# Kernel tuning notes

Measured on AMD Instinct MI355X. Metric: run time of the kernel, lower is better.

## Reference

```python
import jax, jax.numpy as jnp
import numpy as np

IN_F = 512
OUT_F = 512
NOISE_DIM = 128
BATCH = 512
OUT_DIM = IN_F * OUT_F + OUT_F  # 262656
PRIOR_STD = 1.0
PRIOR_SCALE = 1.0
POSTERIOR_SCALE = 1.0


def setup_inputs() -> dict:
    key = jax.random.key(0)
    k1, k2, k3, k4, k5, k6 = jax.random.split(key, 6)
    x = jax.random.normal(k1, (BATCH, IN_F), dtype=jnp.float32)
    prior_x = jax.random.normal(k2, (BATCH, IN_F), dtype=jnp.float32)
    hyper_noise = jax.random.normal(k3, (BATCH, NOISE_DIM), dtype=jnp.float32)
    # hypermodel = nn.Linear(noise_dim, out_dim): kaiming-uniform-ish init approximated by uniform
    bound = 1.0 / np.sqrt(NOISE_DIM)
    hW = jax.random.uniform(k4, (OUT_DIM, NOISE_DIM), jnp.float32, -bound, bound)
    hb = jax.random.uniform(k5, (OUT_DIM,), jnp.float32, -bound, bound)
    # PriorHyperLinear: row-normalized gaussian weight scaled by prior_std (eye), zero bias (prior_mean=0)
    pW = jax.random.normal(k6, (OUT_DIM, NOISE_DIM), dtype=jnp.float32)
    pW = PRIOR_STD * pW / jnp.linalg.norm(pW, axis=1, keepdims=True)
    pb = jnp.zeros((OUT_DIM,), dtype=jnp.float32)
    return {"x": x, "prior_x": prior_x, "hyper_noise": hyper_noise,
            "hW": hW, "hb": hb, "pW": pW, "pb": pb}


def _base_forward(x, params):
    # params: [B, in*out + out] -> per-sample weight [B, in, out], bias [B, out]
    weight = params[:, : IN_F * OUT_F].reshape(-1, IN_F, OUT_F)
    bias = params[:, IN_F * OUT_F:]  # [B, out]
    # bmm(x[:,None,:], weight) + bias -> [B, out]
    return jnp.einsum("bi,bio->bo", x, weight) + bias


def reference(x, prior_x, hyper_noise, hW, hb, pW, pb):
    params = hyper_noise @ hW.T + hb  # [B, out_dim]
    out = _base_forward(x, params)
    prior_params = hyper_noise @ pW.T + pb
    prior_out = _base_forward(prior_x, prior_params)
    return out * POSTERIOR_SCALE + prior_out * PRIOR_SCALE
```

## Files before the change

### kernel.cpp

```cpp
#include <hip/hip_runtime.h>
#include <hip/hip_fp16.h>

#define BATCH 512
#define INF   512
#define OUTF  512
#define ND    128
#define WPART 262144

typedef __attribute__((ext_vector_type(8))) _Float16 half8;
typedef __attribute__((ext_vector_type(2))) _Float16 half2v;
typedef __attribute__((ext_vector_type(4))) float    f32x4;

__device__ inline half8 cvt8(float4 a, float4 b) {
  half2v h0 = __builtin_bit_cast(half2v, __builtin_amdgcn_cvt_pkrtz(a.x, a.y));
  half2v h1 = __builtin_bit_cast(half2v, __builtin_amdgcn_cvt_pkrtz(a.z, a.w));
  half2v h2 = __builtin_bit_cast(half2v, __builtin_amdgcn_cvt_pkrtz(b.x, b.y));
  half2v h3 = __builtin_bit_cast(half2v, __builtin_amdgcn_cvt_pkrtz(b.z, b.w));
  half8 r = { h0[0], h0[1], h1[0], h1[1], h2[0], h2[1], h3[0], h3[1] };
  return r;
}

__global__ void __launch_bounds__(256) transpose_kernel(
    const float* __restrict__ x, const float* __restrict__ px,
    float* __restrict__ xt) {
  __shared__ float t[32][33];
  const float* src = blockIdx.z ? px : x;
  float* dst = xt + ((size_t)blockIdx.z << 18);
  const int bi = blockIdx.x * 32, bb = blockIdx.y * 32;
  const int tx = threadIdx.x & 31, ty = threadIdx.x >> 5;
  #pragma unroll
  for (int r = 0; r < 32; r += 8)
    t[ty + r][tx] = src[(size_t)(bb + ty + r) * 512 + bi + tx];
  __syncthreads();
  #pragma unroll
  for (int r = 0; r < 32; r += 8)
    dst[(size_t)(bi + ty + r) * 512 + bb + tx] = t[tx][ty + r];
}

__global__ void __launch_bounds__(256) tail_kernel(
    const float* __restrict__ hn, const float* __restrict__ hW,
    const float* __restrict__ pW, float* __restrict__ TT) {
  const int bt = blockIdx.x & 7;
  const int bg = blockIdx.x >> 3;
  __shared__ float wsum[64][132];
  __shared__ float hs[32][132];
  {
    int r = threadIdx.x >> 2, seg = threadIdx.x & 3;
    const float4* h4 = (const float4*)(hW + (((size_t)(WPART + bt*64 + r)) << 7) + seg*32);
    const float4* p4 = (const float4*)(pW + (((size_t)(WPART + bt*64 + r)) << 7) + seg*32);
    #pragma unroll
    for (int qq = 0; qq < 8; ++qq) {
      float4 a = h4[qq], b = p4[qq];
      float* d = &wsum[r][seg*32 + qq*4];
      d[0]=a.x+b.x; d[1]=a.y+b.y; d[2]=a.z+b.z; d[3]=a.w+b.w;
    }
    int bb = threadIdx.x >> 3, ch = threadIdx.x & 7;
    const float4* hh = (const float4*)(hn + (((size_t)(bg*32 + bb)) << 7) + ch*16);
    #pragma unroll
    for (int qq = 0; qq < 4; ++qq) {
      float4 a = hh[qq];
      float* d = &hs[bb][ch*16 + qq*4];
      d[0]=a.x; d[1]=a.y; d[2]=a.z; d[3]=a.w;
    }
  }
  __syncthreads();
  const int ol = threadIdx.x & 63, b0 = (threadIdx.x >> 6) * 8;
  float a[8] = {};
  for (int n = 0; n < 128; n += 4) {
    float4 wv = *(const float4*)&wsum[ol][n];
    #pragma unroll
    for (int r = 0; r < 8; ++r) {
      float4 hv = *(const float4*)&hs[b0 + r][n];
      a[r] += hv.x*wv.x + hv.y*wv.y + hv.z*wv.z + hv.w*wv.w;
    }
  }
  #pragma unroll
  for (int r = 0; r < 8; ++r)
    TT[(((size_t)(bg*32 + b0 + r)) << 9) + bt*64 + ol] = a[r];
}

__global__ void __launch_bounds__(1024, 4) gemm_kernel(
    const float* __restrict__ xt, const float* __restrict__ hn,
    const float* __restrict__ hW, const float* __restrict__ pW,
    float* __restrict__ P, int S) {
  const int tid = threadIdx.x;
  const int lane = tid & 63, w = tid >> 6;
  const int l15 = lane & 15, j = lane >> 4;
  const int wrow0 = w << 5;

  const int n0 = blockIdx.x << 6;
  const int q  = blockIdx.y;
  const int spb  = S >> 3;
  const int half = S >> 1;
  const int part = q / half;
  const int rem  = q % half;
  const int nh   = rem / spb;
  const int irange = 512 / spb;
  const int i0   = (rem % spb) * irange;
  const int nst  = irange >> 1;
  const float* srcW = part ? pW : hW;
  const float* xtp  = xt + ((size_t)part << 18);
  const int woff = nh << 5;

  __shared__ half8 ldsW[2][512];

  f32x4 acc[2][4] = {};

  const int o_s = tid >> 4;
  const int g_s = tid & 15;
  const int isub_s = g_s >> 3;
  const size_t colbase = (((size_t)(n0 + o_s)) << 7) + woff + ((g_s & 7) << 2);
  const int wdst = (o_s << 7) + (((((g_s >> 1)) ^ (o_s & 7)) << 4) | ((g_s & 1) << 3));

  half8 hnf[2];
  #pragma unroll
  for (int m = 0; m < 2; ++m) {
    int row = wrow0 + m * 16 + l15;
    const float4* hp = (const float4*)(hn + ((size_t)row << 7) + woff + (j << 3));
    hnf[m] = cvt8(hp[0], hp[1]);
  }

  auto loadW = [&](int ph, float4& rw) {
    int i = i0 + 2 * ph + isub_s;
    rw = *(const float4*)(srcW + ((size_t)i << 16) + colbase);
  };
  auto writeW = [&](int buf, float4 rw) {
    unsigned u0 = __builtin_bit_cast(unsigned, __builtin_amdgcn_cvt_pkrtz(rw.x, rw.y));
    unsigned u1 = __builtin_bit_cast(unsigned, __builtin_amdgcn_cvt_pkrtz(rw.z, rw.w));
    uint2 u; u.x = u0; u.y = u1;
    *(uint2*)((char*)&ldsW[buf][0] + wdst) = u;
  };
  auto loadX = [&](int ph, float4& xq) {
    const float* g = xtp + (((size_t)(i0 + 2 * ph)) << 9) + wrow0 + l15;
    xq.x = g[0];
    xq.y = g[16];
    xq.z = g[512];
    xq.w = g[528];
  };
  auto compute = [&](int buf, float4 xq) {
    const char* bW = (const char*)&ldsW[buf][0];
    #pragma unroll
    for (int kk = 0; kk < 2; ++kk) {
      half8 af[2], bf[4];
      _Float16 t0 = (_Float16)(kk ? xq.z : xq.x);
      _Float16 t1 = (_Float16)(kk ? xq.w : xq.y);
      half8 xb0 = { t0, t0, t0, t0, t0, t0, t0, t0 };
      half8 xb1 = { t1, t1, t1, t1, t1, t1, t1, t1 };
      af[0] = hnf[0] * xb0;
      af[1] = hnf[1] * xb1;
      #pragma unroll
      for (int nn = 0; nn < 4; ++nn) {
        int byte = (((nn << 4) + l15) << 7) + (((((kk << 2) + j)) ^ (l15 & 7)) << 4);
        bf[nn] = *(const half8*)(bW + byte);
      }
      __builtin_amdgcn_s_setprio(1);
      #pragma unroll
      for (int m = 0; m < 2; ++m)
        #pragma unroll
        for (int nn = 0; nn < 4; ++nn)
          acc[m][nn] = __builtin_amdgcn_mfma_f32_16x16x32_f16(
              af[m], bf[nn], acc[m][nn], 0, 0, 0);
      __builtin_amdgcn_s_setprio(0);
    }
  };

  float4 rw0, rw1, rw2, rw3, xq0, xq1, xq2, xq3;
  loadW(0, rw0); loadX(0, xq0);
  loadW(1, rw1); loadX(1, xq1);
  loadW(2, rw2); loadX(2, xq2);
  loadW(3, rw3); loadX(3, xq3);
  writeW(0, rw0);

#define PHASE(p, RWCUR, XQCUR, RWNEXT, BUF)                                \
  {                                                                        \
    asm volatile("s_waitcnt lgkmcnt(0)" ::: "memory");                     \
    __builtin_amdgcn_s_barrier();                                          \
    if ((p) + 4 < nst) loadW((p) + 4, RWCUR);                              \
    compute(BUF, XQCUR);                                                   \
    if ((p) + 4 < nst) loadX((p) + 4, XQCUR);                              \
    if ((p) + 1 < nst) writeW(BUF ^ 1, RWNEXT);                            \
  }

  for (int p = 0; p < nst; p += 4) {
    PHASE(p + 0, rw0, xq0, rw1, 0)
    PHASE(p + 1, rw1, xq1, rw2, 1)
    PHASE(p + 2, rw2, xq2, rw3, 0)
    PHASE(p + 3, rw3, xq3, rw0, 1)
  }
#undef PHASE

  float* outp = P + ((size_t)q << 18);
  #pragma unroll
  for (int m = 0; m < 2; ++m) {
    int row = wrow0 + m * 16 + (j << 2);
    #pragma unroll
    for (int nn = 0; nn < 4; ++nn) {
      int col = n0 + (nn << 4) + l15;
      float* op = outp + (size_t)row * OUTF + col;
      op[0]    = acc[m][nn][0];
      op[512]  = acc[m][nn][1];
      op[1024] = acc[m][nn][2];
      op[1536] = acc[m][nn][3];
    }
  }
}

__global__ void __launch_bounds__(256) finish_kernel(
    const float* __restrict__ P, const float* __restrict__ x,
    const float* __restrict__ hb, const float* __restrict__ TT,
    float* __restrict__ out, int S) {
  const int o  = blockIdx.x * 256 + threadIdx.x;
  const int b0 = blockIdx.y * 2;
  __shared__ float xs[2][512];
  #pragma unroll
  for (int t = 0; t < 4; ++t) {
    int idx = threadIdx.x + t * 256;
    xs[idx >> 9][idx & 511] = x[((size_t)(b0 + (idx >> 9)) << 9) + (idx & 511)];
  }
  __syncthreads();

  const float bias = hb[WPART + o];
  float a0 = bias, a1 = bias;
  #pragma unroll 16
  for (int i = 0; i < 512; ++i) {
    float hv = hb[(i << 9) + o];
    a0 += xs[0][i] * hv;
    a1 += xs[1][i] * hv;
  }
  a0 += TT[((size_t)b0 << 9) + o];
  a1 += TT[((size_t)(b0 + 1) << 9) + o];

  const float* P0 = P + ((size_t)b0 << 9) + o;
  const float* P1 = P0 + 512;
  float t00 = 0, t01 = 0, t10 = 0, t11 = 0;
  #pragma unroll 4
  for (int k = 0; k < S; k += 2) {
    t00 += P0[(size_t)(k)     << 18];
    t01 += P0[(size_t)(k + 1) << 18];
    t10 += P1[(size_t)(k)     << 18];
    t11 += P1[(size_t)(k + 1) << 18];
  }
  out[((size_t)b0 << 9) + o]       = a0 + t00 + t01;
  out[((size_t)(b0 + 1) << 9) + o] = a1 + t10 + t11;
}

extern "C" void kernel_launch(void* const* d_in, const int* in_sizes, int n_in,
                              void* d_out, int out_size, void* d_ws, size_t ws_size,
                              hipStream_t stream) {
  const float* x  = (const float*)d_in[0];
  const float* px = (const float*)d_in[1];
  const float* hn = (const float*)d_in[2];
  const float* hW = (const float*)d_in[3];
  const float* hb = (const float*)d_in[4];
  const float* pW = (const float*)d_in[5];
  float* out = (float*)d_out;
  float* xt  = (float*)d_ws;
  float* TT  = xt + (1 << 19);
  float* P   = TT + (1 << 18);

  int S = 32;
  while (S > 8 && (((size_t)(3 + S)) << 20) > ws_size) S >>= 1;

  transpose_kernel<<<dim3(16, 16, 2), 256, 0, stream>>>(x, px, xt);
  tail_kernel<<<dim3(128), 256, 0, stream>>>(hn, hW, pW, TT);
  gemm_kernel<<<dim3(8, S), dim3(1024), 0, stream>>>(xt, hn, hW, pW, P, S);
  finish_kernel<<<dim3(2, 256), dim3(256), 0, stream>>>(P, x, hb, TT, out, S);
}
```

Measured before the change: 116.3 us.

## Retile MFMA GEMM to 4x2 warp fragments with four i-steps per stage

Each warp now covers a 64-row by 32-column tile (4x2 MFMA fragments) instead of 32x64, and every pipeline stage consumes four input rows i instead of two, which halves the number of barrier-separated stages. The W staging buffer doubles to 1024 half8 per buffer with a new swizzle, and each thread loads 8 contiguous floats per stage. The prefetch depth drops from four to two register stages. The intent is to cut barrier and LDS-read overhead per MFMA, at the cost of more registers and less latency hiding for global loads.

```diff
diff --git a/kernel.cpp b/kernel.cpp
--- a/kernel.cpp
+++ b/kernel.cpp
@@ -19,6 +19,8 @@
   half8 r = { h0[0], h0[1], h1[0], h1[1], h2[0], h2[1], h3[0], h3[1] };
   return r;
 }
+
+struct XQ { float4 k0, k1, k2, k3; };
 
 __global__ void __launch_bounds__(256) transpose_kernel(
     const float* __restrict__ x, const float* __restrict__ px,
@@ -86,7 +88,8 @@
   const int tid = threadIdx.x;
   const int lane = tid & 63, w = tid >> 6;
   const int l15 = lane & 15, j = lane >> 4;
-  const int wrow0 = w << 5;
+  const int wm = w >> 1, wn = w & 1;
+  const int wrow0 = wm << 6;
 
   const int n0 = blockIdx.x << 6;
   const int q  = blockIdx.y;
@@ -97,105 +100,111 @@
   const int nh   = rem / spb;
   const int irange = 512 / spb;
   const int i0   = (rem % spb) * irange;
-  const int nst  = irange >> 1;
+  const int nst  = irange >> 2;
   const float* srcW = part ? pW : hW;
   const float* xtp  = xt + ((size_t)part << 18);
   const int woff = nh << 5;
 
-  __shared__ half8 ldsW[2][512];
-
-  f32x4 acc[2][4] = {};
-
-  const int o_s = tid >> 4;
-  const int g_s = tid & 15;
-  const int isub_s = g_s >> 3;
-  const size_t colbase = (((size_t)(n0 + o_s)) << 7) + woff + ((g_s & 7) << 2);
-  const int wdst = (o_s << 7) + (((((g_s >> 1)) ^ (o_s & 7)) << 4) | ((g_s & 1) << 3));
-
-  half8 hnf[2];
-  #pragma unroll
-  for (int m = 0; m < 2; ++m) {
+  __shared__ half8 ldsW[2][1024];
+
+  f32x4 acc[4][2] = {};
+
+  const int col_s = tid >> 4;
+  const int c_s   = tid & 15;
+  const int isub_s = c_s >> 2;
+  const int nloc_s = (c_s & 3) << 3;
+  const int swz_s  = (c_s & 8) | ((c_s & 7) ^ (col_s & 7));
+  const int wbyte  = (col_s << 8) + (swz_s << 4);
+
+  half8 hnf[4];
+  #pragma unroll
+  for (int m = 0; m < 4; ++m) {
     int row = wrow0 + m * 16 + l15;
     const float4* hp = (const float4*)(hn + ((size_t)row << 7) + woff + (j << 3));
     hnf[m] = cvt8(hp[0], hp[1]);
   }
 
-  auto loadW = [&](int ph, float4& rw) {
-    int i = i0 + 2 * ph + isub_s;
-    rw = *(const float4*)(srcW + ((size_t)i << 16) + colbase);
-  };
-  auto writeW = [&](int buf, float4 rw) {
-    unsigned u0 = __builtin_bit_cast(unsigned, __builtin_amdgcn_cvt_pkrtz(rw.x, rw.y));
-    unsigned u1 = __builtin_bit_cast(unsigned, __builtin_amdgcn_cvt_pkrtz(rw.z, rw.w));
-    uint2 u; u.x = u0; u.y = u1;
-    *(uint2*)((char*)&ldsW[buf][0] + wdst) = u;
-  };
-  auto loadX = [&](int ph, float4& xq) {
-    const float* g = xtp + (((size_t)(i0 + 2 * ph)) << 9) + wrow0 + l15;
-    xq.x = g[0];
-    xq.y = g[16];
-    xq.z = g[512];
-    xq.w = g[528];
-  };
-  auto compute = [&](int buf, float4 xq) {
+  auto loadW = [&](int ph, float4& ra, float4& rb) {
+    int i = i0 + 4 * ph + isub_s;
+    const float* g = srcW + (((size_t)((i << 9) + n0 + col_s)) << 7) + woff + nloc_s;
+    ra = *(const float4*)g;
+    rb = *(const float4*)(g + 4);
+  };
+  auto writeW = [&](int buf, float4 ra, float4 rb) {
+    *(half8*)((char*)&ldsW[buf][0] + wbyte) = cvt8(ra, rb);
+  };
+  auto loadX = [&](int ph, XQ& xq) {
+    const float* g = xtp + (((size_t)(i0 + 4 * ph)) << 9) + wrow0 + l15;
+    xq.k0 = make_float4(g[0],        g[16],        g[32],        g[48]);
+    xq.k1 = make_float4(g[512],      g[528],       g[544],       g[560]);
+    xq.k2 = make_float4(g[1024],     g[1040],      g[1056],      g[1072]);
+    xq.k3 = make_float4(g[1536],     g[1552],      g[1568],      g[1584]);
+  };
+  auto compute = [&](int buf, const XQ& xq) {
     const char* bW = (const char*)&ldsW[buf][0];
     #pragma unroll
-    for (int kk = 0; kk < 2; ++kk) {
-      half8 af[2], bf[4];
-      _Float16 t0 = (_Float16)(kk ? xq.z : xq.x);
-      _Float16 t1 = (_Float16)(kk ? xq.w : xq.y);
-      half8 xb0 = { t0, t0, t0, t0, t0, t0, t0, t0 };
-      half8 xb1 = { t1, t1, t1, t1, t1, t1, t1, t1 };
-      af[0] = hnf[0] * xb0;
-      af[1] = hnf[1] * xb1;
+    for (int kk = 0; kk < 4; ++kk) {
+      float4 xk = kk == 0 ? xq.k0 : kk == 1 ? xq.k1 : kk == 2 ? xq.k2 : xq.k3;
+      half8 bf[2];
       #pragma unroll
-      for (int nn = 0; nn < 4; ++nn) {
-        int byte = (((nn << 4) + l15) << 7) + (((((kk << 2) + j)) ^ (l15 & 7)) << 4);
-        bf[nn] = *(const half8*)(bW + byte);
+      for (int nn = 0; nn < 2; ++nn) {
+        int col = (wn << 5) + (nn << 4) + l15;
+        int ch  = (kk << 2) + j;
+        int swz = (ch & 8) | ((ch & 7) ^ (col & 7));
+        bf[nn] = *(const half8*)(bW + (col << 8) + (swz << 4));
       }
+      _Float16 t0 = (_Float16)xk.x, t1 = (_Float16)xk.y;
+      _Float16 t2 = (_Float16)xk.z, t3 = (_Float16)xk.w;
+      half8 xb0 = { t0,t0,t0,t0,t0,t0,t0,t0 };
+      half8 xb1 = { t1,t1,t1,t1,t1,t1,t1,t1 };
+      half8 xb2 = { t2,t2,t2,t2,t2,t2,t2,t2 };
+      half8 xb3 = { t3,t3,t3,t3,t3,t3,t3,t3 };
+      half8 af0 = hnf[0] * xb0;
+      half8 af1 = hnf[1] * xb1;
+      half8 af2 = hnf[2] * xb2;
+      half8 af3 = hnf[3] * xb3;
       __builtin_amdgcn_s_setprio(1);
       #pragma unroll
-      for (int m = 0; m < 2; ++m)
-        #pragma unroll
-        for (int nn = 0; nn < 4; ++nn)
-          acc[m][nn] = __builtin_amdgcn_mfma_f32_16x16x32_f16(
-              af[m], bf[nn], acc[m][nn], 0, 0, 0);
+      for (int nn = 0; nn < 2; ++nn) {
+        acc[0][nn] = __builtin_amdgcn_mfma_f32_16x16x32_f16(af0, bf[nn], acc[0][nn], 0, 0, 0);
+        acc[1][nn] = __builtin_amdgcn_mfma_f32_16x16x32_f16(af1, bf[nn], acc[1][nn], 0, 0, 0);
+        acc[2][nn] = __builtin_amdgcn_mfma_f32_16x16x32_f16(af2, bf[nn], acc[2][nn], 0, 0, 0);
+        acc[3][nn] = __builtin_amdgcn_mfma_f32_16x16x32_f16(af3, bf[nn], acc[3][nn], 0, 0, 0);
+      }
       __builtin_amdgcn_s_setprio(0);
     }
   };
 
-  float4 rw0, rw1, rw2, rw3, xq0, xq1, xq2, xq3;
-  loadW(0, rw0); loadX(0, xq0);
-  loadW(1, rw1); loadX(1, xq1);
-  loadW(2, rw2); loadX(2, xq2);
-  loadW(3, rw3); loadX(3, xq3);
-  writeW(0, rw0);
-
-#define PHASE(p, RWCUR, XQCUR, RWNEXT, BUF)                                \
-  {                                                                        \
-    asm volatile("s_waitcnt lgkmcnt(0)" ::: "memory");                     \
-    __builtin_amdgcn_s_barrier();                                          \
-    if ((p) + 4 < nst) loadW((p) + 4, RWCUR);                              \
-    compute(BUF, XQCUR);                                                   \
-    if ((p) + 4 < nst) loadX((p) + 4, XQCUR);                              \
-    if ((p) + 1 < nst) writeW(BUF ^ 1, RWNEXT);                            \
-  }
-
-  for (int p = 0; p < nst; p += 4) {
-    PHASE(p + 0, rw0, xq0, rw1, 0)
-    PHASE(p + 1, rw1, xq1, rw2, 1)
-    PHASE(p + 2, rw2, xq2, rw3, 0)
-    PHASE(p + 3, rw3, xq3, rw0, 1)
-  }
-#undef PHASE
+  float4 rwA0, rwA1, rwB0, rwB1;
+  XQ xA, xB;
+  loadW(0, rwA0, rwA1);
+  loadX(0, xA);
+  loadW(1, rwB0, rwB1);
+  writeW(0, rwA0, rwA1);
+
+  for (int p = 0; p < nst; p += 2) {
+    asm volatile("s_waitcnt lgkmcnt(0)" ::: "memory");
+    __builtin_amdgcn_s_barrier();
+    if (p + 2 < nst) loadW(p + 2, rwA0, rwA1);
+    if (p + 1 < nst) loadX(p + 1, xB);
+    compute(0, xA);
+    if (p + 1 < nst) writeW(1, rwB0, rwB1);
+
+    asm volatile("s_waitcnt lgkmcnt(0)" ::: "memory");
+    __builtin_amdgcn_s_barrier();
+    if (p + 3 < nst) loadW(p + 3, rwB0, rwB1);
+    if (p + 2 < nst) loadX(p + 2, xA);
+    if (p + 1 < nst) compute(1, xB);
+    if (p + 2 < nst) writeW(0, rwA0, rwA1);
+  }
 
   float* outp = P + ((size_t)q << 18);
   #pragma unroll
-  for (int m = 0; m < 2; ++m) {
+  for (int m = 0; m < 4; ++m) {
     int row = wrow0 + m * 16 + (j << 2);
     #pragma unroll
-    for (int nn = 0; nn < 4; ++nn) {
-      int col = n0 + (nn << 4) + l15;
+    for (int nn = 0; nn < 2; ++nn) {
+      int col = n0 + (wn << 5) + (nn << 4) + l15;
       float* op = outp + (size_t)row * OUTF + col;
       op[0]    = acc[m][nn][0];
       op[512]  = acc[m][nn][1];
```

Result: slower. 133.3 us (+14.6%).

## Retile gemm to 512-thread blocks with 64-row warps and interleaved x layout

Applied to the files above, without the earlier changes.

The GEMM block shrinks from 1024 to 512 threads. Each warp now covers 64 batch rows by 32 output columns, using 4x2 MFMA tiles instead of 2x4, and twice as many blocks are launched along the column dimension. The transpose kernel now writes x in pairs of consecutive i as float2, so each x load fetches both k-steps with one 8-byte access, and the x prefetch depth drops from 4 to 2 stages. This cuts the number of scalar x loads and registers held, at the cost of loading the W tile from HBM twice as often relative to rows, since each block covers fewer columns.

```diff
diff --git a/kernel.cpp b/kernel.cpp
--- a/kernel.cpp
+++ b/kernel.cpp
@@ -20,12 +20,14 @@
   return r;
 }
 
+struct XR { float2 m0, m1, m2, m3; };
+
 __global__ void __launch_bounds__(256) transpose_kernel(
     const float* __restrict__ x, const float* __restrict__ px,
     float* __restrict__ xt) {
   __shared__ float t[32][33];
   const float* src = blockIdx.z ? px : x;
-  float* dst = xt + ((size_t)blockIdx.z << 18);
+  float2* dst = (float2*)(xt + ((size_t)blockIdx.z << 18));
   const int bi = blockIdx.x * 32, bb = blockIdx.y * 32;
   const int tx = threadIdx.x & 31, ty = threadIdx.x >> 5;
   #pragma unroll
@@ -33,8 +35,11 @@
     t[ty + r][tx] = src[(size_t)(bb + ty + r) * 512 + bi + tx];
   __syncthreads();
   #pragma unroll
-  for (int r = 0; r < 32; r += 8)
-    dst[(size_t)(bi + ty + r) * 512 + bb + tx] = t[tx][ty + r];
+  for (int r = 0; r < 16; r += 8) {
+    int ipl = ty + r;
+    float2 v; v.x = t[tx][2 * ipl]; v.y = t[tx][2 * ipl + 1];
+    dst[(size_t)((bi >> 1) + ipl) * 512 + bb + tx] = v;
+  }
 }
 
 __global__ void __launch_bounds__(256) tail_kernel(
@@ -79,16 +84,16 @@
     TT[(((size_t)(bg*32 + b0 + r)) << 9) + bt*64 + ol] = a[r];
 }
 
-__global__ void __launch_bounds__(1024, 4) gemm_kernel(
+__global__ void __launch_bounds__(512, 4) gemm_kernel(
     const float* __restrict__ xt, const float* __restrict__ hn,
     const float* __restrict__ hW, const float* __restrict__ pW,
     float* __restrict__ P, int S) {
   const int tid = threadIdx.x;
   const int lane = tid & 63, w = tid >> 6;
   const int l15 = lane & 15, j = lane >> 4;
-  const int wrow0 = w << 5;
-
-  const int n0 = blockIdx.x << 6;
+  const int wrow0 = w << 6;
+
+  const int n0 = blockIdx.x << 5;
   const int q  = blockIdx.y;
   const int spb  = S >> 3;
   const int half = S >> 1;
@@ -99,12 +104,13 @@
   const int i0   = (rem % spb) * irange;
   const int nst  = irange >> 1;
   const float* srcW = part ? pW : hW;
-  const float* xtp  = xt + ((size_t)part << 18);
+  const float2* xt2p = (const float2*)(xt + ((size_t)part << 18));
+  const int ip0 = i0 >> 1;
   const int woff = nh << 5;
 
-  __shared__ half8 ldsW[2][512];
-
-  f32x4 acc[2][4] = {};
+  __shared__ half8 ldsW[2][256];
+
+  f32x4 acc[4][2] = {};
 
   const int o_s = tid >> 4;
   const int g_s = tid & 15;
@@ -112,9 +118,9 @@
   const size_t colbase = (((size_t)(n0 + o_s)) << 7) + woff + ((g_s & 7) << 2);
   const int wdst = (o_s << 7) + (((((g_s >> 1)) ^ (o_s & 7)) << 4) | ((g_s & 1) << 3));
 
-  half8 hnf[2];
-  #pragma unroll
-  for (int m = 0; m < 2; ++m) {
+  half8 hnf[4];
+  #pragma unroll
+  for (int m = 0; m < 4; ++m) {
     int row = wrow0 + m * 16 + l15;
     const float4* hp = (const float4*)(hn + ((size_t)row << 7) + woff + (j << 3));
     hnf[m] = cvt8(hp[0], hp[1]);
@@ -130,71 +136,75 @@
     uint2 u; u.x = u0; u.y = u1;
     *(uint2*)((char*)&ldsW[buf][0] + wdst) = u;
   };
-  auto loadX = [&](int ph, float4& xq) {
-    const float* g = xtp + (((size_t)(i0 + 2 * ph)) << 9) + wrow0 + l15;
-    xq.x = g[0];
-    xq.y = g[16];
-    xq.z = g[512];
-    xq.w = g[528];
-  };
-  auto compute = [&](int buf, float4 xq) {
+  auto loadX = [&](int ph, XR& xq) {
+    const float2* g = xt2p + (((size_t)(ip0 + ph)) << 9) + wrow0 + l15;
+    xq.m0 = g[0]; xq.m1 = g[16]; xq.m2 = g[32]; xq.m3 = g[48];
+  };
+  auto compute = [&](int buf, const XR& xq) {
     const char* bW = (const char*)&ldsW[buf][0];
     #pragma unroll
     for (int kk = 0; kk < 2; ++kk) {
-      half8 af[2], bf[4];
-      _Float16 t0 = (_Float16)(kk ? xq.z : xq.x);
-      _Float16 t1 = (_Float16)(kk ? xq.w : xq.y);
-      half8 xb0 = { t0, t0, t0, t0, t0, t0, t0, t0 };
-      half8 xb1 = { t1, t1, t1, t1, t1, t1, t1, t1 };
-      af[0] = hnf[0] * xb0;
-      af[1] = hnf[1] * xb1;
+      half8 bf[2];
       #pragma unroll
-      for (int nn = 0; nn < 4; ++nn) {
-        int byte = (((nn << 4) + l15) << 7) + (((((kk << 2) + j)) ^ (l15 & 7)) << 4);
+      for (int nn = 0; nn < 2; ++nn) {
+        int col = (nn << 4) + l15;
+        int byte = (col << 7) + (((((kk << 2) + j)) ^ (l15 & 7)) << 4);
         bf[nn] = *(const half8*)(bW + byte);
       }
+      _Float16 t0 = (_Float16)(kk ? xq.m0.y : xq.m0.x);
+      _Float16 t1 = (_Float16)(kk ? xq.m1.y : xq.m1.x);
+      _Float16 t2 = (_Float16)(kk ? xq.m2.y : xq.m2.x);
+      _Float16 t3 = (_Float16)(kk ? xq.m3.y : xq.m3.x);
+      half8 xb0 = { t0,t0,t0,t0,t0,t0,t0,t0 };
+      half8 xb1 = { t1,t1,t1,t1,t1,t1,t1,t1 };
+      half8 xb2 = { t2,t2,t2,t2,t2,t2,t2,t2 };
+      half8 xb3 = { t3,t3,t3,t3,t3,t3,t3,t3 };
+      half8 af0 = hnf[0] * xb0;
+      half8 af1 = hnf[1] * xb1;
+      half8 af2 = hnf[2] * xb2;
+      half8 af3 = hnf[3] * xb3;
       __builtin_amdgcn_s_setprio(1);
       #pragma unroll
-      for (int m = 0; m < 2; ++m)
-        #pragma unroll
-        for (int nn = 0; nn < 4; ++nn)
-          acc[m][nn] = __builtin_amdgcn_mfma_f32_16x16x32_f16(
-              af[m], bf[nn], acc[m][nn], 0, 0, 0);
+      for (int nn = 0; nn < 2; ++nn) {
+        acc[0][nn] = __builtin_amdgcn_mfma_f32_16x16x32_f16(af0, bf[nn], acc[0][nn], 0, 0, 0);
+        acc[1][nn] = __builtin_amdgcn_mfma_f32_16x16x32_f16(af1, bf[nn], acc[1][nn], 0, 0, 0);
+        acc[2][nn] = __builtin_amdgcn_mfma_f32_16x16x32_f16(af2, bf[nn], acc[2][nn], 0, 0, 0);
+        acc[3][nn] = __builtin_amdgcn_mfma_f32_16x16x32_f16(af3, bf[nn], acc[3][nn], 0, 0, 0);
+      }
       __builtin_amdgcn_s_setprio(0);
     }
   };
 
-  float4 rw0, rw1, rw2, rw3, xq0, xq1, xq2, xq3;
-  loadW(0, rw0); loadX(0, xq0);
-  loadW(1, rw1); loadX(1, xq1);
-  loadW(2, rw2); loadX(2, xq2);
-  loadW(3, rw3); loadX(3, xq3);
+  float4 rw0, rw1, rw2, rw3;
+  XR xqA, xqB;
+  loadW(0, rw0); loadW(1, rw1); loadW(2, rw2); loadW(3, rw3);
+  loadX(0, xqA); loadX(1, xqB);
   writeW(0, rw0);
 
-#define PHASE(p, RWCUR, XQCUR, RWNEXT, BUF)                                \
+#define PH(p, RWCUR, RWNEXT, BUF, XQ)                                      \
   {                                                                        \
     asm volatile("s_waitcnt lgkmcnt(0)" ::: "memory");                     \
     __builtin_amdgcn_s_barrier();                                          \
     if ((p) + 4 < nst) loadW((p) + 4, RWCUR);                              \
-    compute(BUF, XQCUR);                                                   \
-    if ((p) + 4 < nst) loadX((p) + 4, XQCUR);                              \
+    compute(BUF, XQ);                                                      \
+    if ((p) + 2 < nst) loadX((p) + 2, XQ);                                 \
     if ((p) + 1 < nst) writeW(BUF ^ 1, RWNEXT);                            \
   }
 
   for (int p = 0; p < nst; p += 4) {
-    PHASE(p + 0, rw0, xq0, rw1, 0)
-    PHASE(p + 1, rw1, xq1, rw2, 1)
-    PHASE(p + 2, rw2, xq2, rw3, 0)
-    PHASE(p + 3, rw3, xq3, rw0, 1)
-  }
-#undef PHASE
+    PH(p + 0, rw0, rw1, 0, xqA)
+    PH(p + 1, rw1, rw2, 1, xqB)
+    PH(p + 2, rw2, rw3, 0, xqA)
+    PH(p + 3, rw3, rw0, 1, xqB)
+  }
+#undef PH
 
   float* outp = P + ((size_t)q << 18);
   #pragma unroll
-  for (int m = 0; m < 2; ++m) {
+  for (int m = 0; m < 4; ++m) {
     int row = wrow0 + m * 16 + (j << 2);
     #pragma unroll
-    for (int nn = 0; nn < 4; ++nn) {
+    for (int nn = 0; nn < 2; ++nn) {
       int col = n0 + (nn << 4) + l15;
       float* op = outp + (size_t)row * OUTF + col;
       op[0]    = acc[m][nn][0];
@@ -263,6 +273,6 @@
 
   transpose_kernel<<<dim3(16, 16, 2), 256, 0, stream>>>(x, px, xt);
   tail_kernel<<<dim3(128), 256, 0, stream>>>(hn, hW, pW, TT);
-  gemm_kernel<<<dim3(8, S), dim3(1024), 0, stream>>>(xt, hn, hW, pW, P, S);
+  gemm_kernel<<<dim3(16, S), dim3(512), 0, stream>>>(xt, hn, hW, pW, P, S);
   finish_kernel<<<dim3(2, 256), dim3(256), 0, stream>>>(P, x, hb, TT, out, S);
 }
```

After: 145.8 us. 25.3% more time.

## Double per-stage K depth in gemm pipeline and pair x columns in transpose

Applied to the files above, without the earlier changes.

Each pipeline stage in the GEMM now processes four input rows instead of two. This halves the number of barrier-synchronized stages and doubles the LDS buffer. The transposed x layout is changed to store pairs of i values as float2, so each thread loads x with fewer, wider reads. The cost is more registers held per stage (two float4 W loads per prefetch slot) and more LDS, which may reduce occupancy under the 1024-thread launch bound.

```diff
diff --git a/kernel.cpp b/kernel.cpp
--- a/kernel.cpp
+++ b/kernel.cpp
@@ -20,12 +20,15 @@
   return r;
 }
 
+struct WR  { float4 a, b; };
+struct XR2 { float2 a0, a1, b0, b1; };
+
 __global__ void __launch_bounds__(256) transpose_kernel(
     const float* __restrict__ x, const float* __restrict__ px,
     float* __restrict__ xt) {
   __shared__ float t[32][33];
   const float* src = blockIdx.z ? px : x;
-  float* dst = xt + ((size_t)blockIdx.z << 18);
+  float2* dst = (float2*)(xt + ((size_t)blockIdx.z << 18));
   const int bi = blockIdx.x * 32, bb = blockIdx.y * 32;
   const int tx = threadIdx.x & 31, ty = threadIdx.x >> 5;
   #pragma unroll
@@ -33,8 +36,11 @@
     t[ty + r][tx] = src[(size_t)(bb + ty + r) * 512 + bi + tx];
   __syncthreads();
   #pragma unroll
-  for (int r = 0; r < 32; r += 8)
-    dst[(size_t)(bi + ty + r) * 512 + bb + tx] = t[tx][ty + r];
+  for (int r = 0; r < 16; r += 8) {
+    int ipl = ty + r;
+    float2 v; v.x = t[tx][2 * ipl]; v.y = t[tx][2 * ipl + 1];
+    dst[(size_t)((bi >> 1) + ipl) * 512 + bb + tx] = v;
+  }
 }
 
 __global__ void __launch_bounds__(256) tail_kernel(
@@ -97,12 +103,13 @@
   const int nh   = rem / spb;
   const int irange = 512 / spb;
   const int i0   = (rem % spb) * irange;
-  const int nst  = irange >> 1;
+  const int nst  = irange >> 2;
   const float* srcW = part ? pW : hW;
-  const float* xtp  = xt + ((size_t)part << 18);
+  const float2* xt2p = (const float2*)(xt + ((size_t)part << 18));
+  const int ip0 = i0 >> 1;
   const int woff = nh << 5;
 
-  __shared__ half8 ldsW[2][512];
+  __shared__ half8 ldsW[2][1024];
 
   f32x4 acc[2][4] = {};
 
@@ -110,7 +117,7 @@
   const int g_s = tid & 15;
   const int isub_s = g_s >> 3;
   const size_t colbase = (((size_t)(n0 + o_s)) << 7) + woff + ((g_s & 7) << 2);
-  const int wdst = (o_s << 7) + (((((g_s >> 1)) ^ (o_s & 7)) << 4) | ((g_s & 1) << 3));
+  const int wdstI = (((((g_s >> 1)) ^ (o_s & 7)) << 4) | ((g_s & 1) << 3));
 
   half8 hnf[2];
   #pragma unroll
@@ -120,37 +127,45 @@
     hnf[m] = cvt8(hp[0], hp[1]);
   }
 
-  auto loadW = [&](int ph, float4& rw) {
-    int i = i0 + 2 * ph + isub_s;
-    rw = *(const float4*)(srcW + ((size_t)i << 16) + colbase);
-  };
-  auto writeW = [&](int buf, float4 rw) {
-    unsigned u0 = __builtin_bit_cast(unsigned, __builtin_amdgcn_cvt_pkrtz(rw.x, rw.y));
-    unsigned u1 = __builtin_bit_cast(unsigned, __builtin_amdgcn_cvt_pkrtz(rw.z, rw.w));
-    uint2 u; u.x = u0; u.y = u1;
-    *(uint2*)((char*)&ldsW[buf][0] + wdst) = u;
-  };
-  auto loadX = [&](int ph, float4& xq) {
-    const float* g = xtp + (((size_t)(i0 + 2 * ph)) << 9) + wrow0 + l15;
-    xq.x = g[0];
-    xq.y = g[16];
-    xq.z = g[512];
-    xq.w = g[528];
-  };
-  auto compute = [&](int buf, float4 xq) {
+  auto loadW = [&](int ph, WR& r) {
+    int iA = i0 + 4 * ph + isub_s;
+    r.a = *(const float4*)(srcW + ((size_t)iA << 16) + colbase);
+    r.b = *(const float4*)(srcW + ((size_t)(iA + 2) << 16) + colbase);
+  };
+  auto writeW = [&](int buf, const WR& r) {
+    unsigned ua0 = __builtin_bit_cast(unsigned, __builtin_amdgcn_cvt_pkrtz(r.a.x, r.a.y));
+    unsigned ua1 = __builtin_bit_cast(unsigned, __builtin_amdgcn_cvt_pkrtz(r.a.z, r.a.w));
+    unsigned ub0 = __builtin_bit_cast(unsigned, __builtin_amdgcn_cvt_pkrtz(r.b.x, r.b.y));
+    unsigned ub1 = __builtin_bit_cast(unsigned, __builtin_amdgcn_cvt_pkrtz(r.b.z, r.b.w));
+    char* base = (char*)&ldsW[buf][0] + (o_s << 8) + wdstI;
+    uint2 u0; u0.x = ua0; u0.y = ua1;
+    uint2 u1; u1.x = ub0; u1.y = ub1;
+    *(uint2*)base         = u0;
+    *(uint2*)(base + 128) = u1;
+  };
+  auto loadX = [&](int ph, XR2& xq) {
+    const float2* g = xt2p + (((size_t)(ip0 + 2 * ph)) << 9) + wrow0 + l15;
+    xq.a0 = g[0]; xq.a1 = g[16];
+    xq.b0 = g[512]; xq.b1 = g[528];
+  };
+  auto compute = [&](int buf, const XR2& xq) {
     const char* bW = (const char*)&ldsW[buf][0];
     #pragma unroll
-    for (int kk = 0; kk < 2; ++kk) {
+    for (int kk = 0; kk < 4; ++kk) {
       half8 af[2], bf[4];
-      _Float16 t0 = (_Float16)(kk ? xq.z : xq.x);
-      _Float16 t1 = (_Float16)(kk ? xq.w : xq.y);
-      half8 xb0 = { t0, t0, t0, t0, t0, t0, t0, t0 };
-      half8 xb1 = { t1, t1, t1, t1, t1, t1, t1, t1 };
+      float2 xm0 = (kk & 2) ? xq.b0 : xq.a0;
+      float2 xm1 = (kk & 2) ? xq.b1 : xq.a1;
+      _Float16 t0 = (_Float16)((kk & 1) ? xm0.y : xm0.x);
+      _Float16 t1 = (_Float16)((kk & 1) ? xm1.y : xm1.x);
+      half8 xb0 = { t0,t0,t0,t0,t0,t0,t0,t0 };
+      half8 xb1 = { t1,t1,t1,t1,t1,t1,t1,t1 };
       af[0] = hnf[0] * xb0;
       af[1] = hnf[1] * xb1;
       #pragma unroll
       for (int nn = 0; nn < 4; ++nn) {
-        int byte = (((nn << 4) + l15) << 7) + (((((kk << 2) + j)) ^ (l15 & 7)) << 4);
+        int col  = (nn << 4) + l15;
+        int byte = (col << 8) + ((kk >> 1) << 7)
+                 + (((((kk & 1) << 2) + j) ^ (l15 & 7)) << 4);
         bf[nn] = *(const half8*)(bW + byte);
       }
       __builtin_amdgcn_s_setprio(1);
@@ -164,30 +179,29 @@
     }
   };
 
-  float4 rw0, rw1, rw2, rw3, xq0, xq1, xq2, xq3;
-  loadW(0, rw0); loadX(0, xq0);
-  loadW(1, rw1); loadX(1, xq1);
-  loadW(2, rw2); loadX(2, xq2);
-  loadW(3, rw3); loadX(3, xq3);
-  writeW(0, rw0);
-
-#define PHASE(p, RWCUR, XQCUR, RWNEXT, BUF)                                \
+  WR wr0, wr1, wr2, wr3;
+  XR2 xqA, xqB;
+  loadW(0, wr0); loadW(1, wr1); loadW(2, wr2); loadW(3, wr3);
+  loadX(0, xqA); loadX(1, xqB);
+  writeW(0, wr0);
+
+#define PH(p, WCUR, WNEXT, BUF, XQ)                                        \
   {                                                                        \
     asm volatile("s_waitcnt lgkmcnt(0)" ::: "memory");                     \
     __builtin_amdgcn_s_barrier();                                          \
-    if ((p) + 4 < nst) loadW((p) + 4, RWCUR);                              \
-    compute(BUF, XQCUR);                                                   \
-    if ((p) + 4 < nst) loadX((p) + 4, XQCUR);                              \
-    if ((p) + 1 < nst) writeW(BUF ^ 1, RWNEXT);                            \
+    if ((p) + 4 < nst) loadW((p) + 4, WCUR);                               \
+    compute(BUF, XQ);                                                      \
+    if ((p) + 2 < nst) loadX((p) + 2, XQ);                                 \
+    if ((p) + 1 < nst) writeW(BUF ^ 1, WNEXT);                             \
   }
 
   for (int p = 0; p < nst; p += 4) {
-    PHASE(p + 0, rw0, xq0, rw1, 0)
-    PHASE(p + 1, rw1, xq1, rw2, 1)
-    PHASE(p + 2, rw2, xq2, rw3, 0)
-    PHASE(p + 3, rw3, xq3, rw0, 1)
-  }
-#undef PHASE
+    PH(p + 0, wr0, wr1, 0, xqA)
+    PH(p + 1, wr1, wr2, 1, xqB)
+    PH(p + 2, wr2, wr3, 0, xqA)
+    PH(p + 3, wr3, wr0, 1, xqB)
+  }
+#undef PH
 
   float* outp = P + ((size_t)q << 18);
   #pragma unroll
```

New measurement: 161.2 us. 1.39x slower.
